# Kernel optimization log

Measured on AMD Instinct MI355X. Metric: run time of the kernel, lower is better.

Reference implementation:

```python
import jax, jax.numpy as jnp
import numpy as np

D_MODEL = 256
D_INNER = 512
D_STATE = 16
DT_RANK = 16
D_CONV = 4
N_LAYERS = 2
L2_LAMBDA = 0.01


def _layernorm(x, g, b, eps=1e-5):
    mu = x.mean(-1, keepdims=True)
    var = x.var(-1, keepdims=True)
    return (x - mu) / jnp.sqrt(var + eps) * g + b


def _selective_scan(u, delta, A, Bm, C, D):
    # u, delta: (B, L, di); A: (di, ds); Bm, C: (B, L, ds); D: (di,)
    B_, L, di = u.shape
    ds = A.shape[1]

    def step(s, inp):
        d_t, u_t, b_t, c_t = inp  # (B,di),(B,di),(B,ds),(B,ds)
        dA = jnp.exp(d_t[..., None] * A)                      # (B,di,ds)
        s = s * dA + (d_t * u_t)[..., None] * b_t[:, None, :]  # (B,di,ds)
        y = jnp.einsum('bds,bs->bd', s, c_t)
        return s, y

    s0 = jnp.zeros((B_, di, ds), u.dtype)
    xs = (jnp.swapaxes(delta, 0, 1), jnp.swapaxes(u, 0, 1),
          jnp.swapaxes(Bm, 0, 1), jnp.swapaxes(C, 0, 1))
    _, ys = jax.lax.scan(step, s0, xs)  # ys: (L, B, di)
    return jnp.swapaxes(ys, 0, 1) + u * D


def _mamba_block(x, ng, nb, ipw, cw, cb, xpw, dtw, dtb, A_log, Dp, opw):
    h = _layernorm(x, ng, nb)
    xz = h @ ipw.T                       # (B,L,2*di)
    u, z = xz[..., :D_INNER], xz[..., D_INNER:]
    # causal depthwise conv along time
    uc = jnp.swapaxes(u, 1, 2)           # (B,di,L)
    uc = jax.lax.conv_general_dilated(
        uc, cw, window_strides=(1,), padding=[(D_CONV - 1, 0)],
        feature_group_count=D_INNER,
        dimension_numbers=('NCH', 'OIH', 'NCH')) + cb[None, :, None]
    u = jax.nn.silu(jnp.swapaxes(uc, 1, 2))
    xdbc = u @ xpw.T                     # (B,L,dt_rank+2*ds)
    dt = xdbc[..., :DT_RANK]
    Bm = xdbc[..., DT_RANK:DT_RANK + D_STATE]
    C = xdbc[..., DT_RANK + D_STATE:]
    delta = jax.nn.softplus(dt @ dtw.T + dtb)
    A = -jnp.exp(A_log)
    y = _selective_scan(u, delta, A, Bm, C, Dp)
    y = y * jax.nn.silu(z)
    return x + y @ opw.T


def setup_inputs() -> dict:
    key = jax.random.key(0)
    ks = jax.random.split(key, 24)
    s = 0.05
    inp = {
        'x': jax.random.normal(ks[0], (4, 1024, 768), jnp.float32),
        'in_w': jax.random.normal(ks[1], (D_MODEL, 768), jnp.float32) * s,
        'in_b': jnp.zeros((D_MODEL,), jnp.float32),
        'ln_g': jnp.ones((D_MODEL,), jnp.float32),
        'ln_b': jnp.zeros((D_MODEL,), jnp.float32),
        'blk_ng': jnp.ones((N_LAYERS, D_MODEL), jnp.float32),
        'blk_nb': jnp.zeros((N_LAYERS, D_MODEL), jnp.float32),
        'blk_ipw': jax.random.normal(ks[2], (N_LAYERS, 2 * D_INNER, D_MODEL), jnp.float32) * s,
        'blk_cw': jax.random.normal(ks[3], (N_LAYERS, D_INNER, 1, D_CONV), jnp.float32) * 0.2,
        'blk_cb': jnp.zeros((N_LAYERS, D_INNER), jnp.float32),
        'blk_xpw': jax.random.normal(ks[4], (N_LAYERS, DT_RANK + 2 * D_STATE, D_INNER), jnp.float32) * s,
        'blk_dtw': jax.random.normal(ks[5], (N_LAYERS, D_INNER, DT_RANK), jnp.float32) * s,
        'blk_dtb': jax.random.normal(ks[6], (N_LAYERS, D_INNER), jnp.float32) * 0.1,
        'blk_Alog': jax.random.uniform(ks[7], (N_LAYERS, D_INNER, D_STATE), jnp.float32, 0.0, 1.0),
        'blk_D': jnp.ones((N_LAYERS, D_INNER), jnp.float32),
        'blk_opw': jax.random.normal(ks[8], (N_LAYERS, D_MODEL, D_INNER), jnp.float32) * s,
        'op_w': jax.random.normal(ks[9], (D_MODEL, D_MODEL), jnp.float32) * s,
        'op_b': jnp.zeros((D_MODEL,), jnp.float32),
        'cls_w': jax.random.normal(ks[10], (128, D_MODEL), jnp.float32) * s,
        'cls_b': jnp.zeros((128,), jnp.float32),
    }
    return inp


def reference(x, in_w, in_b, ln_g, ln_b, blk_ng, blk_nb, blk_ipw, blk_cw, blk_cb,
              blk_xpw, blk_dtw, blk_dtb, blk_Alog, blk_D, blk_opw,
              op_w, op_b, cls_w, cls_b):
    h = x @ in_w.T + in_b
    h = _layernorm(h, ln_g, ln_b)
    h = jax.nn.gelu(h, approximate=False)
    # dropout is identity at inference
    for l in range(N_LAYERS):
        h = _mamba_block(h, blk_ng[l], blk_nb[l], blk_ipw[l], blk_cw[l], blk_cb[l],
                         blk_xpw[l], blk_dtw[l], blk_dtb[l], blk_Alog[l], blk_D[l], blk_opw[l])
    h = h @ op_w.T + op_b
    h = jax.nn.gelu(h, approximate=False)
    logits = h @ cls_w.T + cls_b
    l2_loss = L2_LAMBDA * jnp.mean(jnp.linalg.norm(h, axis=-1))
    return logits, l2_loss
```

## Files before the change

kernel.cpp:

```cpp
#include <hip/hip_runtime.h>
#include <hip/hip_bf16.h>
#include <math.h>

typedef __attribute__((ext_vector_type(8))) short frag8;
typedef __attribute__((ext_vector_type(4))) float f32x4;

__device__ __forceinline__ float gelu_exact(float x) {
    return 0.5f * x * (1.0f + erff(x * 0.70710678118654752f));
}
__device__ __forceinline__ float softplus_f(float x) {
    return (x > 20.0f) ? x : log1pf(expf(x));
}
__device__ __forceinline__ float sigmoid_f(float x) {
    return 1.0f / (1.0f + __expf(-x));
}
__device__ __forceinline__ unsigned short bf16bits(float x) {
    __hip_bfloat16 h = __float2bfloat16(x);
    return *(unsigned short*)&h;
}
__device__ __forceinline__ float bf2f(unsigned short u) {
    unsigned int v = ((unsigned int)u) << 16;
    return __builtin_bit_cast(float, v);
}
__device__ __forceinline__ float row_sum16(float x) {
    int t;
    t = __builtin_amdgcn_update_dpp(0, __builtin_bit_cast(int, x), 0x128, 0xf, 0xf, true);
    x += __builtin_bit_cast(float, t);
    t = __builtin_amdgcn_update_dpp(0, __builtin_bit_cast(int, x), 0x124, 0xf, 0xf, true);
    x += __builtin_bit_cast(float, t);
    t = __builtin_amdgcn_update_dpp(0, __builtin_bit_cast(int, x), 0x122, 0xf, 0xf, true);
    x += __builtin_bit_cast(float, t);
    t = __builtin_amdgcn_update_dpp(0, __builtin_bit_cast(int, x), 0x121, 0xf, 0xf, true);
    x += __builtin_bit_cast(float, t);
    return x;
}
__device__ __forceinline__ float prefix_sum64(float x) {
    int t;
    t = __builtin_amdgcn_update_dpp(0, __builtin_bit_cast(int, x), 0x111, 0xf, 0xf, true);
    x += __builtin_bit_cast(float, t);
    t = __builtin_amdgcn_update_dpp(0, __builtin_bit_cast(int, x), 0x112, 0xf, 0xf, true);
    x += __builtin_bit_cast(float, t);
    t = __builtin_amdgcn_update_dpp(0, __builtin_bit_cast(int, x), 0x114, 0xf, 0xf, true);
    x += __builtin_bit_cast(float, t);
    t = __builtin_amdgcn_update_dpp(0, __builtin_bit_cast(int, x), 0x118, 0xf, 0xf, true);
    x += __builtin_bit_cast(float, t);
    t = __builtin_amdgcn_update_dpp(0, __builtin_bit_cast(int, x), 0x142, 0xa, 0xf, true);
    x += __builtin_bit_cast(float, t);
    t = __builtin_amdgcn_update_dpp(0, __builtin_bit_cast(int, x), 0x143, 0xc, 0xf, true);
    x += __builtin_bit_cast(float, t);
    return x;
}

struct CvtArgs {
    const float* src[6];
    unsigned short* dst[6];
    int n4[6];
};
__global__ __launch_bounds__(256)
void cvt_all(CvtArgs a, int total4, const float* __restrict__ Alog,
             float* __restrict__ Ac, float* l2)
{
    int i = blockIdx.x * 256 + threadIdx.x;
    if (i >= total4) {
        int j = i - total4;
        if (j < 16384) Ac[j] = -__expf(Alog[j]);
        if (j == 0) *l2 = 0.0f;
        return;
    }
    int seg = 0;
    while (i >= a.n4[seg]) { i -= a.n4[seg]; seg++; }
    float4 v = reinterpret_cast<const float4*>(a.src[seg])[i];
    ushort4 o;
    o.x = bf16bits(v.x); o.y = bf16bits(v.y); o.z = bf16bits(v.z); o.w = bf16bits(v.w);
    reinterpret_cast<ushort4*>(a.dst[seg])[i] = o;
}

__global__ __launch_bounds__(256)
void gemm_ipw(const unsigned short* __restrict__ A,
              const unsigned short* __restrict__ W,
              float* __restrict__ xzuT,
              unsigned short* __restrict__ szT)
{
    __shared__ __align__(16) unsigned short As[64][40];
    __shared__ __align__(16) unsigned short Bs[64][40];

    const int tid = threadIdx.x;
    const int wid = tid >> 6, lane = tid & 63;
    const int wm = (wid >> 1) * 32, wn = (wid & 1) * 32;
    const int m0 = blockIdx.y * 64, n0 = blockIdx.x * 64;
    const int lrow = lane & 15, quad = lane >> 4;
    const int K = 256;

    const int sm = tid >> 2;
    const int sk = (tid & 3) * 8;

    f32x4 acc[2][2] = {};

    for (int k0 = 0; k0 < K; k0 += 32) {
        float4 av = *reinterpret_cast<const float4*>(A + (size_t)(m0 + sm) * K + k0 + sk);
        *reinterpret_cast<float4*>(&As[sm][sk]) = av;
        float4 bv = *reinterpret_cast<const float4*>(W + (size_t)(n0 + sm) * K + k0 + sk);
        *reinterpret_cast<float4*>(&Bs[sm][sk]) = bv;
        __syncthreads();

        frag8 a0 = *reinterpret_cast<const frag8*>(&As[wm + lrow][quad * 8]);
        frag8 a1 = *reinterpret_cast<const frag8*>(&As[wm + 16 + lrow][quad * 8]);
        frag8 b0 = *reinterpret_cast<const frag8*>(&Bs[wn + lrow][quad * 8]);
        frag8 b1 = *reinterpret_cast<const frag8*>(&Bs[wn + 16 + lrow][quad * 8]);

        acc[0][0] = __builtin_amdgcn_mfma_f32_16x16x32_bf16(a0, b0, acc[0][0], 0, 0, 0);
        acc[0][1] = __builtin_amdgcn_mfma_f32_16x16x32_bf16(a0, b1, acc[0][1], 0, 0, 0);
        acc[1][0] = __builtin_amdgcn_mfma_f32_16x16x32_bf16(a1, b0, acc[1][0], 0, 0, 0);
        acc[1][1] = __builtin_amdgcn_mfma_f32_16x16x32_bf16(a1, b1, acc[1][1], 0, 0, 0);
        __syncthreads();
    }

    const int bb = m0 >> 10;
    const int tb = m0 & 1023;
    #pragma unroll
    for (int mi = 0; mi < 2; mi++) {
        int t4 = tb + wm + mi * 16 + quad * 4;
        #pragma unroll
        for (int nj = 0; nj < 2; nj++) {
            int col = n0 + wn + nj * 16 + lrow;
            if (col < 512) {
                float4 o = { acc[mi][nj][0], acc[mi][nj][1], acc[mi][nj][2], acc[mi][nj][3] };
                *reinterpret_cast<float4*>(xzuT + ((size_t)(bb * 512 + col)) * 1024 + t4) = o;
            } else {
                int z = col - 512;
                ushort4 o;
                float v0 = acc[mi][nj][0], v1 = acc[mi][nj][1], v2 = acc[mi][nj][2], v3 = acc[mi][nj][3];
                o.x = bf16bits(v0 * sigmoid_f(v0));
                o.y = bf16bits(v1 * sigmoid_f(v1));
                o.z = bf16bits(v2 * sigmoid_f(v2));
                o.w = bf16bits(v3 * sigmoid_f(v3));
                *reinterpret_cast<ushort4*>(szT + ((size_t)(bb * 512 + z)) * 1024 + t4) = o;
            }
        }
    }
}

__global__ __launch_bounds__(256)
void gemm_cat(const float* __restrict__ xzuT,
              const unsigned short* __restrict__ W,
              const float* __restrict__ cw, const float* __restrict__ cb,
              float* __restrict__ ucT,
              float* __restrict__ xp0, float* __restrict__ xp123)
{
    __shared__ __align__(16) unsigned short As[64][40];
    __shared__ __align__(16) unsigned short Bs[64][40];

    const int tid = threadIdx.x;
    const int wid = tid >> 6, lane = tid & 63;
    const int wm = (wid >> 1) * 32, wn = (wid & 1) * 32;
    const int kc = blockIdx.x;
    const int m0 = blockIdx.y * 64;
    const int bb = m0 >> 10;
    const int tb = m0 & 1023;
    const int lrow = lane & 15, quad = lane >> 4;
    const int N = 48;

    const int sm = tid >> 2;
    const int sk = (tid & 3) * 8;

    f32x4 acc[2][2] = {};

    for (int k0 = 0; k0 < 128; k0 += 32) {
        #pragma unroll
        for (int p = 0; p < 2; p++) {
            int kk = (tid >> 4) + p * 16;
            int k  = kc * 128 + k0 + kk;
            int mq = tid & 15;
            int tg = tb + mq * 4;
            const float* rowp = xzuT + ((size_t)(bb * 512 + k)) * 1024;
            float4 cur = *reinterpret_cast<const float4*>(rowp + tg);
            float4 prev = {0.f, 0.f, 0.f, 0.f};
            if (tg != 0) prev = *reinterpret_cast<const float4*>(rowp + tg - 4);
            float4 cv = *reinterpret_cast<const float4*>(cw + k * 4);
            float cbv = cb[k];
            float o0 = cbv + cv.x*prev.y + cv.y*prev.z + cv.z*prev.w + cv.w*cur.x;
            float o1 = cbv + cv.x*prev.z + cv.y*prev.w + cv.z*cur.x  + cv.w*cur.y;
            float o2 = cbv + cv.x*prev.w + cv.y*cur.x  + cv.z*cur.y  + cv.w*cur.z;
            float o3 = cbv + cv.x*cur.x  + cv.y*cur.y  + cv.z*cur.z  + cv.w*cur.w;
            o0 *= sigmoid_f(o0); o1 *= sigmoid_f(o1);
            o2 *= sigmoid_f(o2); o3 *= sigmoid_f(o3);
            float4 uo = { o0, o1, o2, o3 };
            *reinterpret_cast<float4*>(ucT + ((size_t)(bb * 512 + k)) * 1024 + tg) = uo;
            As[mq * 4 + 0][kk] = bf16bits(o0);
            As[mq * 4 + 1][kk] = bf16bits(o1);
            As[mq * 4 + 2][kk] = bf16bits(o2);
            As[mq * 4 + 3][kk] = bf16bits(o3);
        }
        float4 bv = {0.f, 0.f, 0.f, 0.f};
        if (sm < N) bv = *reinterpret_cast<const float4*>(W + (size_t)sm * 512 + kc * 128 + k0 + sk);
        *reinterpret_cast<float4*>(&Bs[sm][sk]) = bv;
        __syncthreads();

        frag8 a0 = *reinterpret_cast<const frag8*>(&As[wm + lrow][quad * 8]);
        frag8 a1 = *reinterpret_cast<const frag8*>(&As[wm + 16 + lrow][quad * 8]);
        frag8 b0 = *reinterpret_cast<const frag8*>(&Bs[wn + lrow][quad * 8]);
        frag8 b1 = *reinterpret_cast<const frag8*>(&Bs[wn + 16 + lrow][quad * 8]);

        acc[0][0] = __builtin_amdgcn_mfma_f32_16x16x32_bf16(a0, b0, acc[0][0], 0, 0, 0);
        acc[0][1] = __builtin_amdgcn_mfma_f32_16x16x32_bf16(a0, b1, acc[0][1], 0, 0, 0);
        acc[1][0] = __builtin_amdgcn_mfma_f32_16x16x32_bf16(a1, b0, acc[1][0], 0, 0, 0);
        acc[1][1] = __builtin_amdgcn_mfma_f32_16x16x32_bf16(a1, b1, acc[1][1], 0, 0, 0);
        __syncthreads();
    }

    float* C = (kc == 0) ? xp0 : (xp123 + (size_t)(kc - 1) * 4096 * 48);
    #pragma unroll
    for (int mi = 0; mi < 2; mi++) {
        #pragma unroll
        for (int nj = 0; nj < 2; nj++) {
            int col = wn + nj * 16 + lrow;
            if (col >= N) continue;
            #pragma unroll
            for (int r = 0; r < 4; r++) {
                int row = m0 + wm + mi * 16 + quad * 4 + r;
                C[(size_t)row * N + col] = acc[mi][nj][r];
            }
        }
    }
}

__global__ __launch_bounds__(512)
void rowgemm(const unsigned short* __restrict__ A,
             const float* __restrict__ Af,
             const unsigned short* __restrict__ W,
             const float* __restrict__ bias,
             const float* res,
             const float* g1, const float* b1, int gelu1,
             const float* g2, const float* b2,
             float* outF, unsigned short* outB, float* l2out,
             const unsigned short* clsW, const float* clsB, float* clsOut,
             int K)
{
    __shared__ __align__(16) unsigned short As[16][40];
    __shared__ __align__(16) unsigned short Bs[256][40];
    __shared__ float red[8][16][2];
    __shared__ float sq[16];
    __shared__ __align__(16) unsigned short hb[16][264];

    const int tid = threadIdx.x;
    const int w = tid >> 6, lane = tid & 63;
    const int lrow = lane & 15, quad = lane >> 4;
    const int m0 = blockIdx.x * 16;

    f32x4 acc[2] = {};

    for (int k0 = 0; k0 < K; k0 += 32) {
        if (tid < 64) {
            int r_ = tid >> 2, c8 = (tid & 3) * 8;
            if (Af) {
                float4 v0 = *reinterpret_cast<const float4*>(Af + (size_t)(m0 + r_) * K + k0 + c8);
                float4 v1 = *reinterpret_cast<const float4*>(Af + (size_t)(m0 + r_) * K + k0 + c8 + 4);
                unsigned short* dst = &As[r_][c8];
                dst[0] = bf16bits(v0.x); dst[1] = bf16bits(v0.y);
                dst[2] = bf16bits(v0.z); dst[3] = bf16bits(v0.w);
                dst[4] = bf16bits(v1.x); dst[5] = bf16bits(v1.y);
                dst[6] = bf16bits(v1.z); dst[7] = bf16bits(v1.w);
            } else {
                float4 av = *reinterpret_cast<const float4*>(A + (size_t)(m0 + r_) * K + k0 + c8);
                *reinterpret_cast<float4*>(&As[r_][c8]) = av;
            }
        }
        #pragma unroll
        for (int i = 0; i < 2; i++) {
            int n = (tid >> 2) + i * 128;
            float4 bv = *reinterpret_cast<const float4*>(W + (size_t)n * K + k0 + (tid & 3) * 8);
            *reinterpret_cast<float4*>(&Bs[n][(tid & 3) * 8]) = bv;
        }
        __syncthreads();
        frag8 a = *reinterpret_cast<const frag8*>(&As[lrow][quad * 8]);
        #pragma unroll
        for (int nj = 0; nj < 2; nj++) {
            frag8 b = *reinterpret_cast<const frag8*>(&Bs[w * 32 + nj * 16 + lrow][quad * 8]);
            acc[nj] = __builtin_amdgcn_mfma_f32_16x16x32_bf16(a, b, acc[nj], 0, 0, 0);
        }
        __syncthreads();
    }

    float v[2][4];
    #pragma unroll
    for (int nj = 0; nj < 2; nj++) {
        int col = w * 32 + nj * 16 + lrow;
        #pragma unroll
        for (int r = 0; r < 4; r++) {
            int row = m0 + quad * 4 + r;
            float t = acc[nj][r];
            if (bias) t += bias[col];
            if (res) t += res[(size_t)row * 256 + col];
            v[nj][r] = t;
        }
    }

    if (g1) {
        #pragma unroll
        for (int r = 0; r < 4; r++) {
            float s1 = v[0][r] + v[1][r];
            float s2 = v[0][r]*v[0][r] + v[1][r]*v[1][r];
            s1 = row_sum16(s1); s2 = row_sum16(s2);
            if (lrow == 0) { red[w][quad * 4 + r][0] = s1; red[w][quad * 4 + r][1] = s2; }
        }
        __syncthreads();
        #pragma unroll
        for (int r = 0; r < 4; r++) {
            int rr = quad * 4 + r;
            float t1 = 0.f, t2 = 0.f;
            #pragma unroll
            for (int ww = 0; ww < 8; ww++) { t1 += red[ww][rr][0]; t2 += red[ww][rr][1]; }
            float mu = t1 * (1.0f / 256.0f);
            float var = t2 * (1.0f / 256.0f) - mu * mu;
            float rstd = rsqrtf(var + 1e-5f);
            #pragma unroll
            for (int nj = 0; nj < 2; nj++) {
                int col = w * 32 + nj * 16 + lrow;
                float t = (v[nj][r] - mu) * rstd * g1[col] + b1[col];
                if (gelu1) t = gelu_exact(t);
                v[nj][r] = t;
            }
        }
        __syncthreads();
    } else if (gelu1) {
        #pragma unroll
        for (int nj = 0; nj < 2; nj++)
            #pragma unroll
            for (int r = 0; r < 4; r++)
                v[nj][r] = gelu_exact(v[nj][r]);
    }

    if (outF) {
        #pragma unroll
        for (int nj = 0; nj < 2; nj++) {
            int col = w * 32 + nj * 16 + lrow;
            #pragma unroll
            for (int r = 0; r < 4; r++)
                outF[(size_t)(m0 + quad * 4 + r) * 256 + col] = v[nj][r];
        }
    }

    if (l2out) {
        #pragma unroll
        for (int r = 0; r < 4; r++) {
            float s2 = v[0][r]*v[0][r] + v[1][r]*v[1][r];
            s2 = row_sum16(s2);
            if (lrow == 0) red[w][quad * 4 + r][0] = s2;
        }
        __syncthreads();
        if (tid < 16) {
            float t = 0.f;
            #pragma unroll
            for (int ww = 0; ww < 8; ww++) t += red[ww][tid][0];
            sq[tid] = sqrtf(t);
        }
        __syncthreads();
        if (tid == 0) {
            float a = 0.f;
            #pragma unroll
            for (int i = 0; i < 16; i++) a += sq[i];
            atomicAdd(l2out, a * (0.01f / 4096.0f));
        }
    }

    if (g2) {
        __syncthreads();
        #pragma unroll
        for (int r = 0; r < 4; r++) {
            float s1 = v[0][r] + v[1][r];
            float s2 = v[0][r]*v[0][r] + v[1][r]*v[1][r];
            s1 = row_sum16(s1); s2 = row_sum16(s2);
            if (lrow == 0) { red[w][quad * 4 + r][0] = s1; red[w][quad * 4 + r][1] = s2; }
        }
        __syncthreads();
        #pragma unroll
        for (int r = 0; r < 4; r++) {
            int rr = quad * 4 + r;
            float t1 = 0.f, t2 = 0.f;
            #pragma unroll
            for (int ww = 0; ww < 8; ww++) { t1 += red[ww][rr][0]; t2 += red[ww][rr][1]; }
            float mu = t1 * (1.0f / 256.0f);
            float var = t2 * (1.0f / 256.0f) - mu * mu;
            float rstd = rsqrtf(var + 1e-5f);
            #pragma unroll
            for (int nj = 0; nj < 2; nj++) {
                int col = w * 32 + nj * 16 + lrow;
                outB[(size_t)(m0 + rr) * 256 + col] = bf16bits((v[nj][r] - mu) * rstd * g2[col] + b2[col]);
            }
        }
    } else if (outB) {
        #pragma unroll
        for (int nj = 0; nj < 2; nj++) {
            int col = w * 32 + nj * 16 + lrow;
            #pragma unroll
            for (int r = 0; r < 4; r++)
                outB[(size_t)(m0 + quad * 4 + r) * 256 + col] = bf16bits(v[nj][r]);
        }
    }

    if (clsW) {
        #pragma unroll
        for (int nj = 0; nj < 2; nj++) {
            int col = w * 32 + nj * 16 + lrow;
            #pragma unroll
            for (int r = 0; r < 4; r++)
                hb[quad * 4 + r][col] = bf16bits(v[nj][r]);
        }
        __syncthreads();
        f32x4 cacc = {};
        #pragma unroll
        for (int k0 = 0; k0 < 256; k0 += 32) {
            frag8 a = *reinterpret_cast<const frag8*>(&hb[lrow][k0 + quad * 8]);
            frag8 b = *reinterpret_cast<const frag8*>(clsW + (size_t)(w * 16 + lrow) * 256 + k0 + quad * 8);
            cacc = __builtin_amdgcn_mfma_f32_16x16x32_bf16(a, b, cacc, 0, 0, 0);
        }
        int col = w * 16 + lrow;
        float cb = clsB[col];
        #pragma unroll
        for (int r = 0; r < 4; r++)
            clsOut[(size_t)(m0 + quad * 4 + r) * 128 + col] = cacc[r] + cb;
    }
}

__global__ __launch_bounds__(256)
void dtbc(const float* __restrict__ xp0, const float* __restrict__ xp123,
          const float* __restrict__ dtw,
          const float* __restrict__ dtb, float* __restrict__ dltT,
          float* __restrict__ BT, float* __restrict__ CT)
{
    __shared__ float xd[64][17];
    __shared__ float wS[64][16];
    __shared__ float bS[64];
    const size_t S = (size_t)4096 * 48;
    const int bx = blockIdx.x;
    const int b = bx >> 7;
    const int tt = (bx >> 3) & 15;
    const int dg = bx & 7;
    const int tid = threadIdx.x;
    const int t0 = tt * 64, d0 = dg * 64;

    for (int i = tid; i < 64 * 16; i += 256) {
        int t = i >> 4, k = i & 15;
        size_t off = ((size_t)(b * 1024 + t0 + t)) * 48 + k;
        xd[t][k] = xp0[off] + xp123[off] + xp123[S + off] + xp123[2 * S + off];
    }
    for (int i = tid; i < 64 * 16; i += 256) {
        int dl = i >> 4, k = i & 15;
        wS[dl][k] = dtw[(d0 + dl) * 16 + k];
    }
    if (tid < 64) bS[tid] = dtb[d0 + tid];
    __syncthreads();

    const int tl = tid & 63, w = tid >> 6;
    #pragma unroll 4
    for (int di = 0; di < 16; di++) {
        int dl = w * 16 + di;
        float acc = bS[dl];
        #pragma unroll
        for (int k = 0; k < 16; k++) acc += xd[tl][k] * wS[dl][k];
        dltT[((size_t)(b * 512 + d0 + dl)) * 1024 + t0 + tl] = softplus_f(acc);
    }

    {
        int c = tid >> 6;
        int t = tid & 63;
        int col = dg * 4 + c;
        size_t off = ((size_t)(b * 1024 + t0 + t)) * 48 + 16 + col;
        float v = xp0[off] + xp123[off] + xp123[S + off] + xp123[2 * S + off];
        if (col < 16) BT[((size_t)(b * 16 + col)) * 1024 + t0 + t] = v;
        else          CT[((size_t)(b * 16 + col - 16)) * 1024 + t0 + t] = v;
    }
}

__global__ __launch_bounds__(1024)
void scan_chunked(const float* __restrict__ dltT, const float* __restrict__ ucT,
                  const float* __restrict__ BT, const float* __restrict__ CT,
                  const unsigned short* __restrict__ szT,
                  const float* __restrict__ Ac,
                  const float* __restrict__ Dp,
                  unsigned short* __restrict__ y)
{
    __shared__ float aprod_s[16][64];
    __shared__ float sfin_s[16][64];
    __shared__ float sin_w[16][64];
    __shared__ __align__(16) float ylocal[16][64][4];

    const int j = blockIdx.x;
    const int bid = (j & 7) * 64 + (j >> 3);
    const int b = bid >> 7;
    const int d0 = (bid & 127) * 4;
    const int w = threadIdx.x >> 6;
    const int lane = threadIdx.x & 63;
    const int dsub = lane >> 4, s = lane & 15;
    const int d = d0 + dsub;

    const float Acoef = Ac[d * 16 + s];

    const float4* dp = reinterpret_cast<const float4*>(dltT + ((size_t)(b * 512 + d)) * 1024 + w * 64);
    const float4* up = reinterpret_cast<const float4*>(ucT  + ((size_t)(b * 512 + d)) * 1024 + w * 64);
    const float4* Bp = reinterpret_cast<const float4*>(BT + ((size_t)(b * 16 + s)) * 1024 + w * 64);
    const float4* Cp = reinterpret_cast<const float4*>(CT + ((size_t)(b * 16 + s)) * 1024 + w * 64);

    float st = 0.0f, ap = 1.0f;
    float4 dt4 = dp[0], ut4 = up[0], B4 = Bp[0], C4 = Cp[0];
    #pragma unroll
    for (int q = 0; q < 16; q++) {
        float4 ndt, nut, nB, nC;
        if (q < 15) { ndt = dp[q + 1]; nut = up[q + 1]; nB = Bp[q + 1]; nC = Cp[q + 1]; }
        const float* dtp = (const float*)&dt4;
        const float* utp = (const float*)&ut4;
        const float* Btp = (const float*)&B4;
        const float* Ctp = (const float*)&C4;
        #pragma unroll
        for (int jj = 0; jj < 4; jj++) {
            float dA = __expf(dtp[jj] * Acoef);
            st = st * dA + dtp[jj] * utp[jj] * Btp[jj];
            ap *= dA;
            float part = row_sum16(st * Ctp[jj]);
            if (s == 0) ylocal[w][q * 4 + jj][dsub] = part;
        }
        dt4 = ndt; ut4 = nut; B4 = nB; C4 = nC;
    }
    aprod_s[w][lane] = ap;
    sfin_s[w][lane] = st;
    __syncthreads();

    {
        float pre = 0.0f;
        #pragma unroll
        for (int c = 0; c < 15; c++) {
            float apc = aprod_s[c][lane];
            float sfc = sfin_s[c][lane];
            float cand = sfc + apc * pre;
            pre = (c < w) ? cand : pre;
        }
        sin_w[w][lane] = pre;
    }

    const int t = w * 64 + lane;
    float cums[4];
    #pragma unroll
    for (int dd = 0; dd < 4; dd++)
        cums[dd] = dltT[((size_t)(b * 512 + d0 + dd)) * 1024 + t];
    #pragma unroll
    for (int dd = 0; dd < 4; dd++)
        cums[dd] = prefix_sum64(cums[dd]);

    float4 yl = *reinterpret_cast<const float4*>(&ylocal[w][lane][0]);
    float acc[4] = { yl.x, yl.y, yl.z, yl.w };

    #pragma unroll
    for (int sq = 0; sq < 4; sq++) {
        float Cs[4];
        #pragma unroll
        for (int jj = 0; jj < 4; jj++)
            Cs[jj] = CT[((size_t)(b * 16 + sq * 4 + jj)) * 1024 + t];
        #pragma unroll
        for (int dd = 0; dd < 4; dd++) {
            float4 sin4 = *reinterpret_cast<const float4*>(&sin_w[w][dd * 16 + sq * 4]);
            const float* sp = (const float*)&sin4;
            #pragma unroll
            for (int jj = 0; jj < 4; jj++) {
                float ac = Ac[(d0 + dd) * 16 + sq * 4 + jj];
                acc[dd] += sp[jj] * Cs[jj] * __expf(ac * cums[dd]);
            }
        }
    }

    const size_t row = (size_t)b * 1024 + t;
    #pragma unroll
    for (int dd = 0; dd < 4; dd++) {
        float ut = ucT[((size_t)(b * 512 + d0 + dd)) * 1024 + t];
        float sz = bf2f(szT[((size_t)(b * 512 + d0 + dd)) * 1024 + t]);
        float yv = acc[dd] + ut * Dp[d0 + dd];
        y[row * 512 + d0 + dd] = bf16bits(yv * sz);
    }
}

extern "C" void kernel_launch(void* const* d_in, const int* in_sizes, int n_in,
                              void* d_out, int out_size, void* d_ws, size_t ws_size,
                              hipStream_t stream)
{
    const float* x      = (const float*)d_in[0];
    const float* in_b   = (const float*)d_in[2];
    const float* ln_g   = (const float*)d_in[3];
    const float* ln_b   = (const float*)d_in[4];
    const float* blk_ng  = (const float*)d_in[5];
    const float* blk_nb  = (const float*)d_in[6];
    const float* blk_cw  = (const float*)d_in[8];
    const float* blk_cb  = (const float*)d_in[9];
    const float* blk_dtw = (const float*)d_in[11];
    const float* blk_dtb = (const float*)d_in[12];
    const float* blk_Alog= (const float*)d_in[13];
    const float* blk_D   = (const float*)d_in[14];
    const float* op_b   = (const float*)d_in[17];
    const float* cls_b  = (const float*)d_in[19];
    float* out = (float*)d_out;

    const int BL = 4096;
    float* ws = (float*)d_ws;
    float* h0   = ws;
    float* xzuT = h0 + 1048576;
    float* ucT  = xzuT + 2097152;
    float* xdbc = ucT + 2097152;
    float* dltT = xdbc + 196608;
    float* BT   = dltT + 2097152;
    float* CT   = BT + 65536;
    float* Ac   = CT + 65536;
    unsigned short* szT = (unsigned short*)(Ac + 16384);
    unsigned short* wb  = szT + 2097152;
    unsigned short* hnb = wb + 1130496;
    unsigned short* ybb = hnb + 1048576;
    unsigned short* h0b = hnb;
    float* xp123 = (float*)ybb;
    unsigned short* in_wb  = wb;
    unsigned short* ipw_b  = wb + 196608;
    unsigned short* xpw_b  = wb + 720896;
    unsigned short* opw_b  = wb + 770048;
    unsigned short* op_wb  = wb + 1032192;
    unsigned short* cls_wb = wb + 1097728;

    CvtArgs ca;
    ca.src[0] = (const float*)d_in[1];  ca.dst[0] = in_wb;  ca.n4[0] = 196608 / 4;
    ca.src[1] = (const float*)d_in[7];  ca.dst[1] = ipw_b;  ca.n4[1] = 524288 / 4;
    ca.src[2] = (const float*)d_in[10]; ca.dst[2] = xpw_b;  ca.n4[2] = 49152 / 4;
    ca.src[3] = (const float*)d_in[15]; ca.dst[3] = opw_b;  ca.n4[3] = 262144 / 4;
    ca.src[4] = (const float*)d_in[16]; ca.dst[4] = op_wb;  ca.n4[4] = 65536 / 4;
    ca.src[5] = (const float*)d_in[18]; ca.dst[5] = cls_wb; ca.n4[5] = 32768 / 4;
    int total4 = 1130496 / 4;
    int totalg = total4 + 16384;
    cvt_all<<<(totalg + 255) / 256, 256, 0, stream>>>(ca, total4, blk_Alog, Ac,
                                                      out + (size_t)BL * 128);

    rowgemm<<<256, 512, 0, stream>>>(nullptr, x, in_wb, in_b, nullptr,
                                     ln_g, ln_b, 1,
                                     blk_ng, blk_nb,
                                     h0, hnb, nullptr,
                                     nullptr, nullptr, nullptr, 768);

    for (int l = 0; l < 2; l++) {
        const float* cw   = blk_cw  + (size_t)l * 512 * 4;
        const float* cb   = blk_cb  + l * 512;
        const float* dtw  = blk_dtw + (size_t)l * 512 * 16;
        const float* dtb  = blk_dtb + l * 512;
        const float* Dl   = blk_D   + l * 512;
        const unsigned short* ipwl = ipw_b + (size_t)l * 262144;
        const unsigned short* xpwl = xpw_b + (size_t)l * 24576;
        const unsigned short* opwl = opw_b + (size_t)l * 131072;

        gemm_ipw<<<dim3(16, 64), 256, 0, stream>>>(hnb, ipwl, xzuT, szT);
        gemm_cat<<<dim3(4, 64), 256, 0, stream>>>(xzuT, xpwl, cw, cb, ucT, xdbc, xp123);
        dtbc<<<512, 256, 0, stream>>>(xdbc, xp123, dtw, dtb, dltT, BT, CT);
        scan_chunked<<<512, 1024, 0, stream>>>(dltT, ucT, BT, CT, szT,
                                               Ac + (size_t)l * 8192, Dl, ybb);
        if (l == 0)
            rowgemm<<<256, 512, 0, stream>>>(ybb, nullptr, opwl, nullptr, h0,
                                             nullptr, nullptr, 0,
                                             blk_ng + 256, blk_nb + 256,
                                             h0, hnb, nullptr,
                                             nullptr, nullptr, nullptr, 512);
        else
            rowgemm<<<256, 512, 0, stream>>>(ybb, nullptr, opwl, nullptr, h0,
                                             nullptr, nullptr, 0,
                                             nullptr, nullptr,
                                             nullptr, h0b, nullptr,
                                             nullptr, nullptr, nullptr, 512);
    }

    rowgemm<<<256, 512, 0, stream>>>(h0b, nullptr, op_wb, op_b, nullptr,
                                     nullptr, nullptr, 1,
                                     nullptr, nullptr,
                                     nullptr, nullptr, out + (size_t)BL * 128,
                                     cls_wb, cls_b, out, 256);
}
```

Before: 329.6 us.

## Fuse dtbc into scan via atomic split-K reduction and in-scan delta projection

Removes the dtbc kernel. gemm_cat now accumulates its four K-split partials with atomicAdd directly into per-layer xdt/B/C buffers, which cvt_all zeroes up front. The scan kernel computes delta (dt projection plus softplus) itself and stages delta and u in shared memory. This drops one launch and the round trip of the large dltT buffer, at the cost of float atomics, which make summation order nondeterministic, and extra shared memory and compute in the scan.

```diff
diff --git a/kernel.cpp b/kernel.cpp
--- a/kernel.cpp
+++ b/kernel.cpp
@@ -58,12 +58,20 @@
 };
 __global__ __launch_bounds__(256)
 void cvt_all(CvtArgs a, int total4, const float* __restrict__ Alog,
-             float* __restrict__ Ac, float* l2)
+             float* __restrict__ Ac, float* __restrict__ Z, int zquads, float* l2)
 {
     int i = blockIdx.x * 256 + threadIdx.x;
     if (i >= total4) {
         int j = i - total4;
-        if (j < 16384) Ac[j] = -__expf(Alog[j]);
+        if (j < 16384) {
+            Ac[j] = -__expf(Alog[j]);
+        } else {
+            int z = j - 16384;
+            if (z < zquads) {
+                float4 zero = {0.f, 0.f, 0.f, 0.f};
+                reinterpret_cast<float4*>(Z)[z] = zero;
+            }
+        }
         if (j == 0) *l2 = 0.0f;
         return;
     }
@@ -145,7 +153,7 @@
               const unsigned short* __restrict__ W,
               const float* __restrict__ cw, const float* __restrict__ cb,
               float* __restrict__ ucT,
-              float* __restrict__ xp0, float* __restrict__ xp123)
+              float* __restrict__ xdt, float* __restrict__ BT, float* __restrict__ CT)
 {
     __shared__ __align__(16) unsigned short As[64][40];
     __shared__ __align__(16) unsigned short Bs[64][40];
@@ -208,7 +216,6 @@
         __syncthreads();
     }
 
-    float* C = (kc == 0) ? xp0 : (xp123 + (size_t)(kc - 1) * 4096 * 48);
     #pragma unroll
     for (int mi = 0; mi < 2; mi++) {
         #pragma unroll
@@ -217,8 +224,14 @@
             if (col >= N) continue;
             #pragma unroll
             for (int r = 0; r < 4; r++) {
-                int row = m0 + wm + mi * 16 + quad * 4 + r;
-                C[(size_t)row * N + col] = acc[mi][nj][r];
+                int trow = tb + wm + mi * 16 + quad * 4 + r;
+                float v = acc[mi][nj][r];
+                if (col < 16)
+                    atomicAdd(&xdt[((size_t)(bb * 1024 + trow)) * 16 + col], v);
+                else if (col < 32)
+                    atomicAdd(&BT[((size_t)(bb * 16 + col - 16)) * 1024 + trow], v);
+                else
+                    atomicAdd(&CT[((size_t)(bb * 16 + col - 32)) * 1024 + trow], v);
             }
         }
     }
@@ -422,58 +435,10 @@
     }
 }
 
-__global__ __launch_bounds__(256)
-void dtbc(const float* __restrict__ xp0, const float* __restrict__ xp123,
-          const float* __restrict__ dtw,
-          const float* __restrict__ dtb, float* __restrict__ dltT,
-          float* __restrict__ BT, float* __restrict__ CT)
-{
-    __shared__ float xd[64][17];
-    __shared__ float wS[64][16];
-    __shared__ float bS[64];
-    const size_t S = (size_t)4096 * 48;
-    const int bx = blockIdx.x;
-    const int b = bx >> 7;
-    const int tt = (bx >> 3) & 15;
-    const int dg = bx & 7;
-    const int tid = threadIdx.x;
-    const int t0 = tt * 64, d0 = dg * 64;
-
-    for (int i = tid; i < 64 * 16; i += 256) {
-        int t = i >> 4, k = i & 15;
-        size_t off = ((size_t)(b * 1024 + t0 + t)) * 48 + k;
-        xd[t][k] = xp0[off] + xp123[off] + xp123[S + off] + xp123[2 * S + off];
-    }
-    for (int i = tid; i < 64 * 16; i += 256) {
-        int dl = i >> 4, k = i & 15;
-        wS[dl][k] = dtw[(d0 + dl) * 16 + k];
-    }
-    if (tid < 64) bS[tid] = dtb[d0 + tid];
-    __syncthreads();
-
-    const int tl = tid & 63, w = tid >> 6;
-    #pragma unroll 4
-    for (int di = 0; di < 16; di++) {
-        int dl = w * 16 + di;
-        float acc = bS[dl];
-        #pragma unroll
-        for (int k = 0; k < 16; k++) acc += xd[tl][k] * wS[dl][k];
-        dltT[((size_t)(b * 512 + d0 + dl)) * 1024 + t0 + tl] = softplus_f(acc);
-    }
-
-    {
-        int c = tid >> 6;
-        int t = tid & 63;
-        int col = dg * 4 + c;
-        size_t off = ((size_t)(b * 1024 + t0 + t)) * 48 + 16 + col;
-        float v = xp0[off] + xp123[off] + xp123[S + off] + xp123[2 * S + off];
-        if (col < 16) BT[((size_t)(b * 16 + col)) * 1024 + t0 + t] = v;
-        else          CT[((size_t)(b * 16 + col - 16)) * 1024 + t0 + t] = v;
-    }
-}
-
 __global__ __launch_bounds__(1024)
-void scan_chunked(const float* __restrict__ dltT, const float* __restrict__ ucT,
+void scan_chunked(const float* __restrict__ xdt,
+                  const float* __restrict__ dtw, const float* __restrict__ dtb,
+                  const float* __restrict__ ucT,
                   const float* __restrict__ BT, const float* __restrict__ CT,
                   const unsigned short* __restrict__ szT,
                   const float* __restrict__ Ac,
@@ -484,6 +449,8 @@
     __shared__ float sfin_s[16][64];
     __shared__ float sin_w[16][64];
     __shared__ __align__(16) float ylocal[16][64][4];
+    __shared__ __align__(16) float dltS[4][1032];
+    __shared__ __align__(16) float ucS[4][1032];
 
     const int j = blockIdx.x;
     const int bid = (j & 7) * 64 + (j >> 3);
@@ -493,20 +460,44 @@
     const int lane = threadIdx.x & 63;
     const int dsub = lane >> 4, s = lane & 15;
     const int d = d0 + dsub;
+    const int t = w * 64 + lane;
 
     const float Acoef = Ac[d * 16 + s];
 
-    const float4* dp = reinterpret_cast<const float4*>(dltT + ((size_t)(b * 512 + d)) * 1024 + w * 64);
-    const float4* up = reinterpret_cast<const float4*>(ucT  + ((size_t)(b * 512 + d)) * 1024 + w * 64);
+    {
+        int dd = lane >> 4, tq = (lane & 15) * 4;
+        float4 v = *reinterpret_cast<const float4*>(ucT + ((size_t)(b * 512 + d0 + dd)) * 1024 + w * 64 + tq);
+        *reinterpret_cast<float4*>(&ucS[dd][w * 64 + tq]) = v;
+    }
+    {
+        const float* xr = xdt + ((size_t)(b * 1024) + t) * 16;
+        float4 x0 = *reinterpret_cast<const float4*>(xr + 0);
+        float4 x1 = *reinterpret_cast<const float4*>(xr + 4);
+        float4 x2 = *reinterpret_cast<const float4*>(xr + 8);
+        float4 x3 = *reinterpret_cast<const float4*>(xr + 12);
+        #pragma unroll
+        for (int dd = 0; dd < 4; dd++) {
+            const float* wt = dtw + (size_t)(d0 + dd) * 16;
+            float a2 = dtb[d0 + dd]
+                + x0.x * wt[0]  + x0.y * wt[1]  + x0.z * wt[2]  + x0.w * wt[3]
+                + x1.x * wt[4]  + x1.y * wt[5]  + x1.z * wt[6]  + x1.w * wt[7]
+                + x2.x * wt[8]  + x2.y * wt[9]  + x2.z * wt[10] + x2.w * wt[11]
+                + x3.x * wt[12] + x3.y * wt[13] + x3.z * wt[14] + x3.w * wt[15];
+            dltS[dd][t] = softplus_f(a2);
+        }
+    }
+
     const float4* Bp = reinterpret_cast<const float4*>(BT + ((size_t)(b * 16 + s)) * 1024 + w * 64);
     const float4* Cp = reinterpret_cast<const float4*>(CT + ((size_t)(b * 16 + s)) * 1024 + w * 64);
 
     float st = 0.0f, ap = 1.0f;
-    float4 dt4 = dp[0], ut4 = up[0], B4 = Bp[0], C4 = Cp[0];
+    float4 B4 = Bp[0], C4 = Cp[0];
     #pragma unroll
     for (int q = 0; q < 16; q++) {
-        float4 ndt, nut, nB, nC;
-        if (q < 15) { ndt = dp[q + 1]; nut = up[q + 1]; nB = Bp[q + 1]; nC = Cp[q + 1]; }
+        float4 nB, nC;
+        if (q < 15) { nB = Bp[q + 1]; nC = Cp[q + 1]; }
+        float4 dt4 = *reinterpret_cast<const float4*>(&dltS[dsub][w * 64 + q * 4]);
+        float4 ut4 = *reinterpret_cast<const float4*>(&ucS[dsub][w * 64 + q * 4]);
         const float* dtp = (const float*)&dt4;
         const float* utp = (const float*)&ut4;
         const float* Btp = (const float*)&B4;
@@ -519,7 +510,7 @@
             float part = row_sum16(st * Ctp[jj]);
             if (s == 0) ylocal[w][q * 4 + jj][dsub] = part;
         }
-        dt4 = ndt; ut4 = nut; B4 = nB; C4 = nC;
+        B4 = nB; C4 = nC;
     }
     aprod_s[w][lane] = ap;
     sfin_s[w][lane] = st;
@@ -537,11 +528,10 @@
         sin_w[w][lane] = pre;
     }
 
-    const int t = w * 64 + lane;
     float cums[4];
     #pragma unroll
     for (int dd = 0; dd < 4; dd++)
-        cums[dd] = dltT[((size_t)(b * 512 + d0 + dd)) * 1024 + t];
+        cums[dd] = dltS[dd][t];
     #pragma unroll
     for (int dd = 0; dd < 4; dd++)
         cums[dd] = prefix_sum64(cums[dd]);
@@ -570,7 +560,7 @@
     const size_t row = (size_t)b * 1024 + t;
     #pragma unroll
     for (int dd = 0; dd < 4; dd++) {
-        float ut = ucT[((size_t)(b * 512 + d0 + dd)) * 1024 + t];
+        float ut = ucS[dd][t];
         float sz = bf2f(szT[((size_t)(b * 512 + d0 + dd)) * 1024 + t]);
         float yv = acc[dd] + ut * Dp[d0 + dd];
         y[row * 512 + d0 + dd] = bf16bits(yv * sz);
@@ -602,17 +592,15 @@
     float* h0   = ws;
     float* xzuT = h0 + 1048576;
     float* ucT  = xzuT + 2097152;
-    float* xdbc = ucT + 2097152;
-    float* dltT = xdbc + 196608;
-    float* BT   = dltT + 2097152;
-    float* CT   = BT + 65536;
-    float* Ac   = CT + 65536;
+    float* xdt  = ucT + 2097152;
+    float* BT   = xdt + 131072;
+    float* CT   = BT + 131072;
+    float* Ac   = CT + 131072;
     unsigned short* szT = (unsigned short*)(Ac + 16384);
     unsigned short* wb  = szT + 2097152;
     unsigned short* hnb = wb + 1130496;
     unsigned short* ybb = hnb + 1048576;
     unsigned short* h0b = hnb;
-    float* xp123 = (float*)ybb;
     unsigned short* in_wb  = wb;
     unsigned short* ipw_b  = wb + 196608;
     unsigned short* xpw_b  = wb + 720896;
@@ -628,8 +616,10 @@
     ca.src[4] = (const float*)d_in[16]; ca.dst[4] = op_wb;  ca.n4[4] = 65536 / 4;
     ca.src[5] = (const float*)d_in[18]; ca.dst[5] = cls_wb; ca.n4[5] = 32768 / 4;
     int total4 = 1130496 / 4;
-    int totalg = total4 + 16384;
+    int zquads = 393216 / 4;
+    int totalg = total4 + 16384 + zquads;
     cvt_all<<<(totalg + 255) / 256, 256, 0, stream>>>(ca, total4, blk_Alog, Ac,
+                                                      xdt, zquads,
                                                       out + (size_t)BL * 128);
 
     rowgemm<<<256, 512, 0, stream>>>(nullptr, x, in_wb, in_b, nullptr,
@@ -647,11 +637,13 @@
         const unsigned short* ipwl = ipw_b + (size_t)l * 262144;
         const unsigned short* xpwl = xpw_b + (size_t)l * 24576;
         const unsigned short* opwl = opw_b + (size_t)l * 131072;
+        float* xdtl = xdt + (size_t)l * 65536;
+        float* BTl  = BT  + (size_t)l * 65536;
+        float* CTl  = CT  + (size_t)l * 65536;
 
         gemm_ipw<<<dim3(16, 64), 256, 0, stream>>>(hnb, ipwl, xzuT, szT);
-        gemm_cat<<<dim3(4, 64), 256, 0, stream>>>(xzuT, xpwl, cw, cb, ucT, xdbc, xp123);
-        dtbc<<<512, 256, 0, stream>>>(xdbc, xp123, dtw, dtb, dltT, BT, CT);
-        scan_chunked<<<512, 1024, 0, stream>>>(dltT, ucT, BT, CT, szT,
+        gemm_cat<<<dim3(4, 64), 256, 0, stream>>>(xzuT, xpwl, cw, cb, ucT, xdtl, BTl, CTl);
+        scan_chunked<<<512, 1024, 0, stream>>>(xdtl, dtw, dtb, ucT, BTl, CTl, szT,
                                                Ac + (size_t)l * 8192, Dl, ybb);
         if (l == 0)
             rowgemm<<<256, 512, 0, stream>>>(ybb, nullptr, opwl, nullptr, h0,
```

Measured after the change: 306.4 us. -7.0%, faster.
